# Kernel tuning notes

Measured on AMD Instinct MI355X. Metric: run time of the kernel, lower is better.

Reference implementation:

```python
import jax, jax.numpy as jnp
import numpy as np

N_SRC = 200000
N_DST = 50000
N_EDGES = 1600000
D_IN = 256
D_OUT = 16


def setup_inputs() -> dict:
    key = jax.random.key(0)
    k1, k2, k3, k4, k5 = jax.random.split(key, 5)
    x = jax.random.normal(k1, (N_SRC, D_IN), dtype=jnp.float32)
    W = jax.random.normal(k2, (D_IN, D_OUT), dtype=jnp.float32) / np.sqrt(D_IN)
    b = jnp.zeros((D_OUT,), dtype=jnp.float32)
    edge_src = jax.random.randint(k3, (N_EDGES,), 0, N_SRC, dtype=jnp.int64)
    edge_dst = jax.random.randint(k4, (N_EDGES,), 0, N_DST, dtype=jnp.int64)
    res_n_id = jax.random.randint(k5, (N_DST,), 0, N_SRC, dtype=jnp.int64)
    return {"x": x, "W": W, "b": b, "edge_src": edge_src,
            "edge_dst": edge_dst, "res_n_id": res_n_id}


def reference(x, W, b, edge_src, edge_dst, res_n_id):
    n_src = x.shape[0]
    n_dst = res_n_id.shape[0]
    # Linear transform first (small out dim keeps edge-level traffic low).
    x_lin = x @ W                                   # [n_src, d_out]
    ones = jnp.ones(edge_src.shape, dtype=x.dtype)
    deg_src = jax.ops.segment_sum(ones, edge_src, num_segments=n_src)
    deg_dst = jax.ops.segment_sum(ones, edge_dst, num_segments=n_dst)
    # GCN symmetric normalization with self-loops (sampled bipartite block).
    norm = jax.lax.rsqrt((deg_src[edge_src] + 1.0) * (deg_dst[edge_dst] + 1.0))
    msgs = norm[:, None] * x_lin[edge_src]          # [E, d_out] irregular gather
    agg = jax.ops.segment_sum(msgs, edge_dst, num_segments=n_dst)
    # Self-loop term uses the gathered target-node features x[res_n_id].
    self_term = x_lin[res_n_id] / (deg_dst + 1.0)[:, None]
    out = agg + self_term + b                       # [n_dst, d_out]
    return jax.nn.log_softmax(out, axis=1)
```

## Files before the change

### kernel.cpp

```cpp
#include <hip/hip_runtime.h>
#include <hip/hip_bf16.h>

#define D_IN   256
#define D_OUT  16

__device__ __forceinline__ void acc4(float4& a, float xs, const float4& wv) {
  a.x += xs * wv.x; a.y += xs * wv.y; a.z += xs * wv.z; a.w += xs * wv.w;
}

__global__ __launch_bounds__(256) void xlin_kernel(
    const float* __restrict__ x, const float* __restrict__ W,
    float* __restrict__ xlin, int n_src, int total_waves) {
  const int kg = threadIdx.x & 15;
  const int cg = (threadIdx.x >> 4) & 3;
  const int wv = threadIdx.x >> 6;
  const int gw = blockIdx.x * 4 + wv;

  float4 wf[4][4];
#pragma unroll
  for (int j = 0; j < 4; ++j)
#pragma unroll
    for (int jj = 0; jj < 4; ++jj) {
      int r = 4 * kg + 64 * j + jj;
      wf[j][jj] = *reinterpret_cast<const float4*>(W + r * D_OUT + cg * 4);
    }

  const int npairs = n_src >> 1;
  for (int p = gw; p < npairs; p += total_waves) {
    const int r0 = 2 * p, r1 = 2 * p + 1;
    float4 xv0[4], xv1[4];
#pragma unroll
    for (int j = 0; j < 4; ++j) {
      xv0[j] = *reinterpret_cast<const float4*>(x + (size_t)r0 * D_IN + (kg + 16 * j) * 4);
      xv1[j] = *reinterpret_cast<const float4*>(x + (size_t)r1 * D_IN + (kg + 16 * j) * 4);
    }
    float4 a0 = make_float4(0.f, 0.f, 0.f, 0.f);
    float4 a1 = make_float4(0.f, 0.f, 0.f, 0.f);
#pragma unroll
    for (int j = 0; j < 4; ++j) {
      acc4(a0, xv0[j].x, wf[j][0]); acc4(a1, xv1[j].x, wf[j][0]);
      acc4(a0, xv0[j].y, wf[j][1]); acc4(a1, xv1[j].y, wf[j][1]);
      acc4(a0, xv0[j].z, wf[j][2]); acc4(a1, xv1[j].z, wf[j][2]);
      acc4(a0, xv0[j].w, wf[j][3]); acc4(a1, xv1[j].w, wf[j][3]);
    }
#pragma unroll
    for (int off = 1; off < 16; off <<= 1) {
      a0.x += __shfl_xor(a0.x, off, 16); a0.y += __shfl_xor(a0.y, off, 16);
      a0.z += __shfl_xor(a0.z, off, 16); a0.w += __shfl_xor(a0.w, off, 16);
      a1.x += __shfl_xor(a1.x, off, 16); a1.y += __shfl_xor(a1.y, off, 16);
      a1.z += __shfl_xor(a1.z, off, 16); a1.w += __shfl_xor(a1.w, off, 16);
    }
    if (kg == 0) {
      *reinterpret_cast<float4*>(xlin + (size_t)r0 * D_OUT + cg * 4) = a0;
      *reinterpret_cast<float4*>(xlin + (size_t)r1 * D_OUT + cg * 4) = a1;
    }
  }
}

__global__ __launch_bounds__(256) void deg_kernel(
    const int* __restrict__ es, const int* __restrict__ ed,
    float* __restrict__ deg_src, float* __restrict__ deg_dst,
    int n_edges, int stride) {
  int e = blockIdx.x * 256 + threadIdx.x;
  if (e >= n_edges) return;
  int s = es[(size_t)e * stride];
  int d = ed[(size_t)e * stride];
  atomicAdd(&deg_src[s], 1.0f);
  atomicAdd(&deg_dst[d], 1.0f);
}

__global__ __launch_bounds__(256) void edge_kernel(
    const int* __restrict__ es, const int* __restrict__ ed,
    const float* __restrict__ xlin,
    const float* __restrict__ deg_src, const float* __restrict__ deg_dst,
    float* __restrict__ agg, int n_edges, int stride) {
  int t = blockIdx.x * 256 + threadIdx.x;
  int e = t >> 4;
  int c = t & 15;
  if (e >= n_edges) return;
  int s = es[(size_t)e * stride];
  int d = ed[(size_t)e * stride];
  float norm = rsqrtf((deg_src[s] + 1.0f) * (deg_dst[d] + 1.0f));
  float v = norm * xlin[(size_t)s * D_OUT + c];
  atomicAdd(&agg[(size_t)d * D_OUT + c], v);
}

__global__ __launch_bounds__(256) void finalize_kernel(
    const float* __restrict__ xlin, const int* __restrict__ rn,
    const float* __restrict__ deg_dst, const float* __restrict__ b,
    float* __restrict__ out, int n_dst, int stride) {
  int t = blockIdx.x * 256 + threadIdx.x;
  int row = t >> 4;
  int c = t & 15;
  if (row >= n_dst) return;
  int r = rn[(size_t)row * stride];
  float v = out[(size_t)row * D_OUT + c]
          + xlin[(size_t)r * D_OUT + c] / (deg_dst[row] + 1.0f)
          + b[c];
  float m = v;
#pragma unroll
  for (int off = 1; off < 16; off <<= 1) m = fmaxf(m, __shfl_xor(m, off, 16));
  float ex = expf(v - m);
  float sum = ex;
#pragma unroll
  for (int off = 1; off < 16; off <<= 1) sum += __shfl_xor(sum, off, 16);
  out[(size_t)row * D_OUT + c] = v - m - logf(sum);
}

extern "C" void kernel_launch(void* const* d_in, const int* in_sizes, int n_in,
                              void* d_out, int out_size, void* d_ws, size_t ws_size,
                              hipStream_t stream) {
  const float* x  = (const float*)d_in[0];
  const float* W  = (const float*)d_in[1];
  const float* b  = (const float*)d_in[2];
  const int*   es = (const int*)d_in[3];
  const int*   ed = (const int*)d_in[4];
  const int*   rn = (const int*)d_in[5];
  float* out = (float*)d_out;

  const int n_src = in_sizes[0] / D_IN;
  const int n_dst = out_size / D_OUT;

  int stride_e = 1, n_e = in_sizes[3];
  if (in_sizes[3] == 3200000) { stride_e = 2; n_e = 1600000; }
  int stride_r = 1;
  if (in_sizes[5] == 2 * n_dst) { stride_r = 2; }

  float* xlin    = (float*)d_ws;
  float* deg_src = xlin + (size_t)n_src * D_OUT;
  float* deg_dst = deg_src + n_src;

  (void)hipMemsetAsync(deg_src, 0, (size_t)(n_src + n_dst) * sizeof(float), stream);
  (void)hipMemsetAsync(d_out, 0, (size_t)out_size * sizeof(float), stream);

  {
    const int grid = 1024;
    xlin_kernel<<<grid, 256, 0, stream>>>(x, W, xlin, n_src, grid * 4);
  }
  {
    int grid = (n_e + 255) / 256;
    deg_kernel<<<grid, 256, 0, stream>>>(es, ed, deg_src, deg_dst, n_e, stride_e);
  }
  {
    long long threads = (long long)n_e * D_OUT;
    int grid = (int)((threads + 255) / 256);
    edge_kernel<<<grid, 256, 0, stream>>>(es, ed, xlin, deg_src, deg_dst, out, n_e, stride_e);
  }
  {
    int threads = n_dst * D_OUT;
    int grid = (threads + 255) / 256;
    finalize_kernel<<<grid, 256, 0, stream>>>(xlin, rn, deg_dst, b, out, n_dst, stride_r);
  }
}
```

Measured before the change: 602.0 us.

## Fuse source-degree count into xlin kernel and defer dst normalization to finalize

The source-degree atomic counting moves into the tail of the x@W kernel, which removes the separate degree kernel launch. The destination-degree count is now done inside the edge scatter kernel by one lane per edge. Because the dst normalization factor is constant per destination row, it is factored out of the sum and applied in finalize. The xlin grid is doubled. The edge kernel gains an extra atomic per edge and the sum is now reordered relative to the reference.

```diff
diff --git a/kernel.cpp b/kernel.cpp
--- a/kernel.cpp
+++ b/kernel.cpp
@@ -8,13 +8,16 @@
   a.x += xs * wv.x; a.y += xs * wv.y; a.z += xs * wv.z; a.w += xs * wv.w;
 }
 
-__global__ __launch_bounds__(256) void xlin_kernel(
+__global__ __launch_bounds__(256) void xlin_deg_kernel(
     const float* __restrict__ x, const float* __restrict__ W,
-    float* __restrict__ xlin, int n_src, int total_waves) {
+    float* __restrict__ xlin, const int* __restrict__ es,
+    float* __restrict__ deg_src,
+    int n_src, int n_edges, int stride, int nblocks) {
   const int kg = threadIdx.x & 15;
   const int cg = (threadIdx.x >> 4) & 3;
   const int wv = threadIdx.x >> 6;
   const int gw = blockIdx.x * 4 + wv;
+  const int total_waves = nblocks * 4;
 
   float4 wf[4][4];
 #pragma unroll
@@ -55,34 +58,27 @@
       *reinterpret_cast<float4*>(xlin + (size_t)r1 * D_OUT + cg * 4) = a1;
     }
   }
-}
 
-__global__ __launch_bounds__(256) void deg_kernel(
-    const int* __restrict__ es, const int* __restrict__ ed,
-    float* __restrict__ deg_src, float* __restrict__ deg_dst,
-    int n_edges, int stride) {
-  int e = blockIdx.x * 256 + threadIdx.x;
-  if (e >= n_edges) return;
-  int s = es[(size_t)e * stride];
-  int d = ed[(size_t)e * stride];
-  atomicAdd(&deg_src[s], 1.0f);
-  atomicAdd(&deg_dst[d], 1.0f);
+  for (int e = blockIdx.x * 256 + threadIdx.x; e < n_edges; e += nblocks * 256) {
+    int s = es[(size_t)e * stride];
+    atomicAdd(&deg_src[s], 1.0f);
+  }
 }
 
 __global__ __launch_bounds__(256) void edge_kernel(
     const int* __restrict__ es, const int* __restrict__ ed,
-    const float* __restrict__ xlin,
-    const float* __restrict__ deg_src, const float* __restrict__ deg_dst,
-    float* __restrict__ agg, int n_edges, int stride) {
+    const float* __restrict__ xlin, const float* __restrict__ deg_src,
+    float* __restrict__ m, float* __restrict__ deg_dst,
+    int n_edges, int stride) {
   int t = blockIdx.x * 256 + threadIdx.x;
   int e = t >> 4;
   int c = t & 15;
   if (e >= n_edges) return;
   int s = es[(size_t)e * stride];
   int d = ed[(size_t)e * stride];
-  float norm = rsqrtf((deg_src[s] + 1.0f) * (deg_dst[d] + 1.0f));
-  float v = norm * xlin[(size_t)s * D_OUT + c];
-  atomicAdd(&agg[(size_t)d * D_OUT + c], v);
+  float v = rsqrtf(deg_src[s] + 1.0f) * xlin[(size_t)s * D_OUT + c];
+  atomicAdd(&m[(size_t)d * D_OUT + c], v);
+  if (c == 0) atomicAdd(&deg_dst[d], 1.0f);
 }
 
 __global__ __launch_bounds__(256) void finalize_kernel(
@@ -94,17 +90,18 @@
   int c = t & 15;
   if (row >= n_dst) return;
   int r = rn[(size_t)row * stride];
-  float v = out[(size_t)row * D_OUT + c]
-          + xlin[(size_t)r * D_OUT + c] / (deg_dst[row] + 1.0f)
+  float dd = deg_dst[row];
+  float v = out[(size_t)row * D_OUT + c] * rsqrtf(dd + 1.0f)
+          + xlin[(size_t)r * D_OUT + c] / (dd + 1.0f)
           + b[c];
-  float m = v;
+  float mx = v;
 #pragma unroll
-  for (int off = 1; off < 16; off <<= 1) m = fmaxf(m, __shfl_xor(m, off, 16));
-  float ex = expf(v - m);
+  for (int off = 1; off < 16; off <<= 1) mx = fmaxf(mx, __shfl_xor(mx, off, 16));
+  float ex = expf(v - mx);
   float sum = ex;
 #pragma unroll
   for (int off = 1; off < 16; off <<= 1) sum += __shfl_xor(sum, off, 16);
-  out[(size_t)row * D_OUT + c] = v - m - logf(sum);
+  out[(size_t)row * D_OUT + c] = v - mx - logf(sum);
 }
 
 extern "C" void kernel_launch(void* const* d_in, const int* in_sizes, int n_in,
@@ -134,17 +131,15 @@
   (void)hipMemsetAsync(d_out, 0, (size_t)out_size * sizeof(float), stream);
 
   {
-    const int grid = 1024;
-    xlin_kernel<<<grid, 256, 0, stream>>>(x, W, xlin, n_src, grid * 4);
-  }
-  {
-    int grid = (n_e + 255) / 256;
-    deg_kernel<<<grid, 256, 0, stream>>>(es, ed, deg_src, deg_dst, n_e, stride_e);
+    const int grid = 2048;
+    xlin_deg_kernel<<<grid, 256, 0, stream>>>(x, W, xlin, es, deg_src,
+                                              n_src, n_e, stride_e, grid);
   }
   {
     long long threads = (long long)n_e * D_OUT;
     int grid = (int)((threads + 255) / 256);
-    edge_kernel<<<grid, 256, 0, stream>>>(es, ed, xlin, deg_src, deg_dst, out, n_e, stride_e);
+    edge_kernel<<<grid, 256, 0, stream>>>(es, ed, xlin, deg_src, out, deg_dst,
+                                          n_e, stride_e);
   }
   {
     int threads = n_dst * D_OUT;
```

Measured after the change: 513.3 us. 14.7% less time.
